# Performance work log

Measured on AMD Instinct MI355X. Metric: run time of the kernel, lower is better.

The kernel has to match this reference:

```python
import jax, jax.numpy as jnp
import numpy as np

B, N, D, M, H = 8, 576, 512, 16, 8
DH = D // H
K = int(D * 0.1)  # sparsity_ratio=0.1 -> k=51
EPS = 1e-5


def setup_inputs() -> dict:
    key = jax.random.key(0)
    ks = jax.random.split(key, 12)
    s = 0.02
    return {
        "F_clean": jax.random.normal(ks[0], (B, N, D), jnp.float32),
        "in_proj_w": jax.random.normal(ks[1], (3 * D, D), jnp.float32) * s,
        "in_proj_b": jnp.zeros((3 * D,), jnp.float32),
        "out_proj_w": jax.random.normal(ks[2], (D, D), jnp.float32) * s,
        "out_proj_b": jnp.zeros((D,), jnp.float32),
        "w1": jax.random.normal(ks[3], (D, D), jnp.float32) * s,
        "b1": jnp.zeros((D,), jnp.float32),
        "ln_g": jnp.ones((D,), jnp.float32),
        "ln_b": jnp.zeros((D,), jnp.float32),
        "w2": jax.random.normal(ks[4], (M, D), jnp.float32) * s,
        "b2": jnp.zeros((M,), jnp.float32),
        "templates": jax.random.normal(ks[5], (M, D), jnp.float32),
    }


def reference(F_clean, in_proj_w, in_proj_b, out_proj_w, out_proj_b,
              w1, b1, ln_g, ln_b, w2, b2, templates):
    # --- self attention (torch MultiheadAttention, batch_first, eval mode) ---
    qkv = F_clean @ in_proj_w.T + in_proj_b              # [B,N,3D]
    q, k_, v = jnp.split(qkv, 3, axis=-1)
    def heads(t):
        return t.reshape(B, N, H, DH).transpose(0, 2, 1, 3)  # [B,H,N,dh]
    q, k_, v = heads(q), heads(k_), heads(v)
    scores = jnp.einsum('bhqd,bhkd->bhqk', q, k_) / jnp.sqrt(jnp.float32(DH))
    attn = jax.nn.softmax(scores, axis=-1)
    o = jnp.einsum('bhqk,bhkd->bhqd', attn, v).transpose(0, 2, 1, 3).reshape(B, N, D)
    attn_out = o @ out_proj_w.T + out_proj_b

    F_enh = F_clean + attn_out

    # --- decompose_mlp: Linear -> LayerNorm -> GELU(exact) -> Linear ---
    h = F_enh @ w1.T + b1
    mu = jnp.mean(h, axis=-1, keepdims=True)
    var = jnp.var(h, axis=-1, keepdims=True)
    h = (h - mu) / jnp.sqrt(var + EPS) * ln_g + ln_b
    h = jax.nn.gelu(h, approximate=False)
    components = h @ w2.T + b2                           # [B,N,M]

    # --- outer product: Q[b,n,d,m] = F[b,n,d] * templates[m,d] * comp[b,n,m] ---
    Q = F_clean[:, :, :, None] * templates.T[None, None, :, :] * components[:, :, None, :]

    # --- top-k sparsify along D for each (b,n,m) row ---
    Qr = Q.transpose(0, 1, 3, 2).reshape(B * N * M, D)
    _, topk_idx = jax.lax.top_k(jnp.abs(Qr), K)
    rows = jnp.arange(B * N * M)[:, None]
    mask = jnp.zeros_like(Qr).at[rows, topk_idx].set(1.0)
    Q_sparse = (Qr * mask).reshape(B, N, M, D).transpose(0, 1, 3, 2)
    return Q_sparse
```

## Files before the change

kernel.cpp:

```cpp
#include <hip/hip_runtime.h>
#include <math.h>

#define NNB   576
#define BNR   4608
#define KSEL  51

typedef unsigned short u16;
typedef __attribute__((ext_vector_type(8))) short bf16x8;
typedef __attribute__((ext_vector_type(4))) float f32x4;

__device__ __forceinline__ u16 f2bf(float f) {
    unsigned u = __float_as_uint(f);
    return (u16)((u + 0x8000u) >> 16);
}
__device__ __forceinline__ unsigned pack2(float a, float b) {
    unsigned ua = __float_as_uint(a), ub = __float_as_uint(b);
    return ((ua + 0x8000u) >> 16) | ((ub + 0x8000u) & 0xffff0000u);
}
__device__ __forceinline__ void load_lds16(const void* gp, void* lp) {
    __builtin_amdgcn_global_load_lds((const __attribute__((address_space(1))) void*)gp,
                                     (__attribute__((address_space(3))) void*)lp, 16, 0, 0);
}
__device__ __forceinline__ int dpp_red_add_i(int v) {
    v += __builtin_amdgcn_update_dpp(0, v, 0x111, 0xf, 0xf, true);
    v += __builtin_amdgcn_update_dpp(0, v, 0x112, 0xf, 0xf, true);
    v += __builtin_amdgcn_update_dpp(0, v, 0x114, 0xf, 0xf, true);
    v += __builtin_amdgcn_update_dpp(0, v, 0x118, 0xf, 0xf, true);
    v += __builtin_amdgcn_update_dpp(0, v, 0x142, 0xa, 0xf, true);
    v += __builtin_amdgcn_update_dpp(0, v, 0x143, 0xc, 0xf, true);
    return __builtin_amdgcn_readlane(v, 63);
}
__device__ __forceinline__ float dpp_red_add_f(float x) {
    x += __int_as_float(__builtin_amdgcn_update_dpp(0, __float_as_int(x), 0x111, 0xf, 0xf, true));
    x += __int_as_float(__builtin_amdgcn_update_dpp(0, __float_as_int(x), 0x112, 0xf, 0xf, true));
    x += __int_as_float(__builtin_amdgcn_update_dpp(0, __float_as_int(x), 0x114, 0xf, 0xf, true));
    x += __int_as_float(__builtin_amdgcn_update_dpp(0, __float_as_int(x), 0x118, 0xf, 0xf, true));
    x += __int_as_float(__builtin_amdgcn_update_dpp(0, __float_as_int(x), 0x142, 0xa, 0xf, true));
    x += __int_as_float(__builtin_amdgcn_update_dpp(0, __float_as_int(x), 0x143, 0xc, 0xf, true));
    return __int_as_float(__builtin_amdgcn_readlane(__float_as_int(x), 63));
}

__global__ __launch_bounds__(256)
void cast_bf16(const float* __restrict__ F, const float* __restrict__ ipw,
               const float* __restrict__ opw, const float* __restrict__ w1,
               u16* __restrict__ Fb, u16* __restrict__ ipwb,
               u16* __restrict__ opwb, u16* __restrict__ w1b)
{
    size_t i4 = ((size_t)blockIdx.x * 256 + threadIdx.x) * 4;
    const float* src; u16* dst; size_t off;
    if      (i4 < 2359296) { src = F;   dst = Fb;   off = i4; }
    else if (i4 < 3145728) { src = ipw; dst = ipwb; off = i4 - 2359296; }
    else if (i4 < 3407872) { src = opw; dst = opwb; off = i4 - 3145728; }
    else                   { src = w1;  dst = w1b;  off = i4 - 3407872; }
    float4 v = *(const float4*)(src + off);
    uint2 o; o.x = pack2(v.x, v.y); o.y = pack2(v.z, v.w);
    *(uint2*)(dst + off) = o;
}

template<bool RESID, bool OUT_BF16, bool QSCALE>
__global__ __launch_bounds__(256)
void gemm_mfma64(const u16* __restrict__ A, const u16* __restrict__ Bw,
                 const float* __restrict__ bias, const float* __restrict__ res,
                 void* __restrict__ Cv, int Mr, int Nc, int Kd)
{
    __shared__ uint4 As4[512];
    __shared__ uint4 Bs4[1024];
    const int tid = threadIdx.x;
    const int lane = tid & 63, w = tid >> 6;
    const int wu = __builtin_amdgcn_readfirstlane(w);
    const int r16 = lane & 15, quad = lane >> 4;
    const int r0 = blockIdx.y << 6, c0 = blockIdx.x << 7;

    const u16* pA[2]; const u16* pB[4];
    #pragma unroll
    for (int rd = 0; rd < 2; ++rd) {
        const int c = (rd << 8) + tid;
        const int kb = c >> 8, g = (c >> 6) & 3, rr = (c >> 2) & 15, q = c & 3;
        pA[rd] = A + (size_t)(r0 + (g << 4) + rr) * Kd + (kb << 5) + (q << 3);
    }
    #pragma unroll
    for (int rd = 0; rd < 4; ++rd) {
        const int c = (rd << 8) + tid;
        const int kb = c >> 9, g = (c >> 6) & 7, rr = (c >> 2) & 15, q = c & 3;
        pB[rd] = Bw + (size_t)(c0 + (g << 4) + rr) * Kd + (kb << 5) + (q << 3);
    }

    f32x4 acc[4][2];
    #pragma unroll
    for (int i = 0; i < 4; ++i)
        #pragma unroll
        for (int j = 0; j < 2; ++j) acc[i][j] = (f32x4){0.f, 0.f, 0.f, 0.f};

    for (int kk = 0; kk < Kd; kk += 64) {
        __syncthreads();
        #pragma unroll
        for (int rd = 0; rd < 2; ++rd)
            load_lds16(pA[rd] + kk, (void*)(As4 + (rd << 8) + (wu << 6)));
        #pragma unroll
        for (int rd = 0; rd < 4; ++rd)
            load_lds16(pB[rd] + kk, (void*)(Bs4 + (rd << 8) + (wu << 6)));
        __syncthreads();
        #pragma unroll
        for (int kb = 0; kb < 2; ++kb) {
            bf16x8 af[4], bfr[2];
            #pragma unroll
            for (int i = 0; i < 4; ++i)
                af[i] = *(const bf16x8*)&As4[((kb * 4 + i) << 6) + (r16 << 2) + quad];
            #pragma unroll
            for (int j = 0; j < 2; ++j)
                bfr[j] = *(const bf16x8*)&Bs4[((kb * 8 + (w << 1) + j) << 6) + (r16 << 2) + quad];
            #pragma unroll
            for (int i = 0; i < 4; ++i)
                #pragma unroll
                for (int j = 0; j < 2; ++j)
                    acc[i][j] = __builtin_amdgcn_mfma_f32_16x16x32_bf16(af[i], bfr[j], acc[i][j], 0, 0, 0);
        }
    }

    float bcol[2], scl[2];
    #pragma unroll
    for (int j = 0; j < 2; ++j) {
        const int col = c0 + (w << 5) + (j << 4) + r16;
        bcol[j] = bias[col];
        scl[j] = (QSCALE && col < 512) ? 0.180336880111120426f : 1.0f;
    }
    #pragma unroll
    for (int i = 0; i < 4; ++i) {
        #pragma unroll
        for (int reg = 0; reg < 4; ++reg) {
            const int row = r0 + (i << 4) + (quad << 2) + reg;
            const size_t base = (size_t)row * Nc;
            #pragma unroll
            for (int j = 0; j < 2; ++j) {
                const int col = c0 + (w << 5) + (j << 4) + r16;
                float v = acc[i][j][reg] + bcol[j];
                if (RESID) v += res[base + col];
                if (QSCALE) v *= scl[j];
                if (OUT_BF16) ((u16*)Cv)[base + col] = f2bf(v);
                else          ((float*)Cv)[base + col] = v;
            }
        }
    }
}

template<bool RESID, bool OUT_BF16>
__global__ __launch_bounds__(256)
void gemm_6464(const u16* __restrict__ A, const u16* __restrict__ Bw,
               const float* __restrict__ bias, const float* __restrict__ res,
               void* __restrict__ Cv, int Mr, int Nc, int Kd)
{
    __shared__ uint4 As4[512];
    __shared__ uint4 Bs4[512];
    const int tid = threadIdx.x;
    const int lane = tid & 63, w = tid >> 6;
    const int wu = __builtin_amdgcn_readfirstlane(w);
    const int r16 = lane & 15, quad = lane >> 4;
    const int wy = w >> 1, wx = w & 1;
    const int r0 = blockIdx.y << 6, c0 = blockIdx.x << 6;

    const u16* pA[2]; const u16* pB[2];
    #pragma unroll
    for (int rd = 0; rd < 2; ++rd) {
        const int c = (rd << 8) + tid;
        const int kb = c >> 8, g = (c >> 6) & 3, rr = (c >> 2) & 15, q = c & 3;
        const int row = (g << 4) + rr;
        const int koff = (kb << 5) + (q << 3);
        pA[rd] = A  + (size_t)(r0 + row) * Kd + koff;
        pB[rd] = Bw + (size_t)(c0 + row) * Kd + koff;
    }

    f32x4 acc[2][2];
    #pragma unroll
    for (int i = 0; i < 2; ++i)
        #pragma unroll
        for (int j = 0; j < 2; ++j) acc[i][j] = (f32x4){0.f, 0.f, 0.f, 0.f};

    for (int kk = 0; kk < Kd; kk += 64) {
        __syncthreads();
        #pragma unroll
        for (int rd = 0; rd < 2; ++rd) {
            load_lds16(pA[rd] + kk, (void*)(As4 + (rd << 8) + (wu << 6)));
            load_lds16(pB[rd] + kk, (void*)(Bs4 + (rd << 8) + (wu << 6)));
        }
        __syncthreads();
        #pragma unroll
        for (int kb = 0; kb < 2; ++kb) {
            bf16x8 af[2], bfr[2];
            #pragma unroll
            for (int i = 0; i < 2; ++i)
                af[i] = *(const bf16x8*)&As4[((kb * 4 + (wy << 1) + i) << 6) + (r16 << 2) + quad];
            #pragma unroll
            for (int j = 0; j < 2; ++j)
                bfr[j] = *(const bf16x8*)&Bs4[((kb * 4 + (wx << 1) + j) << 6) + (r16 << 2) + quad];
            #pragma unroll
            for (int i = 0; i < 2; ++i)
                #pragma unroll
                for (int j = 0; j < 2; ++j)
                    acc[i][j] = __builtin_amdgcn_mfma_f32_16x16x32_bf16(af[i], bfr[j], acc[i][j], 0, 0, 0);
        }
    }

    float bcol[2];
    #pragma unroll
    for (int j = 0; j < 2; ++j) bcol[j] = bias[c0 + (wx << 5) + (j << 4) + r16];
    #pragma unroll
    for (int i = 0; i < 2; ++i) {
        #pragma unroll
        for (int reg = 0; reg < 4; ++reg) {
            const int row = r0 + (wy << 5) + (i << 4) + (quad << 2) + reg;
            const size_t base = (size_t)row * Nc;
            #pragma unroll
            for (int j = 0; j < 2; ++j) {
                const int col = c0 + (wx << 5) + (j << 4) + r16;
                float v = acc[i][j][reg] + bcol[j];
                if (RESID) v += res[base + col];
                if (OUT_BF16) ((u16*)Cv)[base + col] = f2bf(v);
                else          ((float*)Cv)[base + col] = v;
            }
        }
    }
}

__global__ __launch_bounds__(256)
void attn_mfma(const u16* __restrict__ qkv, u16* __restrict__ obuf)
{
    __shared__ uint4 Qf[512];
    __shared__ uint4 Kf[512];
    __shared__ u16  Vfs[4096];
    __shared__ u16  Pfs[4096];
    const int tid = threadIdx.x;
    const int lane = tid & 63, w = tid >> 6;
    const int wu = __builtin_amdgcn_readfirstlane(w);
    const int r16 = lane & 15, quad = lane >> 4;
    const int b = blockIdx.y >> 3, h = blockIdx.y & 7;
    const int i0 = blockIdx.x << 6;
    const u16* qb = qkv + (size_t)b * NNB * 1536 + h * 64;

    #pragma unroll
    for (int s = 0; s < 2; ++s) {
        const int linear = (s << 8) + tid;
        const int r = linear >> 3, q7 = linear & 7;
        uint4 v = *(const uint4*)(qb + (size_t)(i0 + r) * 1536 + (q7 << 3));
        Qf[(((q7 >> 2) * 4 + (r >> 4)) << 6) + ((r & 15) << 2) + (q7 & 3)] = v;
    }
    const u16* pK[2];
    #pragma unroll
    for (int rd = 0; rd < 2; ++rd) {
        const int c = (rd << 8) + tid;
        const int kb = c >> 8, g = (c >> 6) & 3, rr = (c >> 2) & 15, q = c & 3;
        pK[rd] = qb + 512 + (size_t)((g << 4) + rr) * 1536 + (kb << 5) + (q << 3);
    }
    const int vp = tid >> 3, vq7 = tid & 7;
    const int vj = vp << 1;
    const int vjl2 = (vj & 7) >> 1, vjq = (vj >> 3) & 3, vjkb = vj >> 5;

    float l_i[4] = {0.f, 0.f, 0.f, 0.f};
    f32x4 accO[4];
    #pragma unroll
    for (int f = 0; f < 4; ++f) accO[f] = (f32x4){0.f, 0.f, 0.f, 0.f};

    for (int j0 = 0; j0 < NNB; j0 += 64) {
        const u16* vbase = qb + 1024 + (size_t)(j0 + vj) * 1536 + (vq7 << 3);
        uint4 vA = *(const uint4*)vbase;
        uint4 vB = *(const uint4*)(vbase + 1536);
        __syncthreads();
        load_lds16(pK[0] + (size_t)j0 * 1536, (void*)(Kf + (wu << 6)));
        load_lds16(pK[1] + (size_t)j0 * 1536, (void*)(Kf + 256 + (wu << 6)));
        {
            const u16* ea = (const u16*)&vA;
            const u16* eb = (const u16*)&vB;
            unsigned* V32 = (unsigned*)Vfs;
            #pragma unroll
            for (int e = 0; e < 8; ++e) {
                const int d = (vq7 << 3) + e;
                const int g = d >> 4;
                const int ch = ((vjkb * 4 + g) << 6) + ((((d & 15) << 2) + vjq) ^ g);
                V32[(ch << 2) + vjl2] = (unsigned)ea[e] | ((unsigned)eb[e] << 16);
            }
        }
        __syncthreads();

        f32x4 accS[4];
        #pragma unroll
        for (int f = 0; f < 4; ++f) accS[f] = (f32x4){0.f, 0.f, 0.f, 0.f};
        #pragma unroll
        for (int kb = 0; kb < 2; ++kb) {
            bf16x8 aq = *(const bf16x8*)&Qf[((kb * 4 + w) << 6) + (r16 << 2) + quad];
            #pragma unroll
            for (int f = 0; f < 4; ++f) {
                bf16x8 bk = *(const bf16x8*)&Kf[((kb * 4 + f) << 6) + (r16 << 2) + quad];
                accS[f] = __builtin_amdgcn_mfma_f32_16x16x32_bf16(aq, bk, accS[f], 0, 0, 0);
            }
        }
        #pragma unroll
        for (int reg = 0; reg < 4; ++reg) {
            const float s0 = exp2f(accS[0][reg]);
            const float s1 = exp2f(accS[1][reg]);
            const float s2 = exp2f(accS[2][reg]);
            const float s3 = exp2f(accS[3][reg]);
            l_i[reg] += (s0 + s1) + (s2 + s3);
            const int m = (quad << 2) + reg;
            const int sm = ((m & 3) << 2) + (m >> 2);
            const float pv[4] = {s0, s1, s2, s3};
            #pragma unroll
            for (int f = 0; f < 4; ++f) {
                const int k = (f << 4) + r16;
                const int ch = (((k >> 5) * 4 + w) << 6) + (((k >> 3) & 3) << 4) + sm;
                Pfs[(ch << 3) + (k & 7)] = f2bf(pv[f]);
            }
        }
        #pragma unroll
        for (int kb = 0; kb < 2; ++kb) {
            bf16x8 ap = *(const bf16x8*)&Pfs[((((kb * 4 + w) << 6) + (quad << 4) + ((r16 & 3) << 2) + (r16 >> 2)) << 3)];
            #pragma unroll
            for (int f = 0; f < 4; ++f) {
                bf16x8 bv = *(const bf16x8*)&Vfs[((((kb * 4 + f) << 6) + (((r16 << 2) + quad) ^ f)) << 3)];
                accO[f] = __builtin_amdgcn_mfma_f32_16x16x32_bf16(ap, bv, accO[f], 0, 0, 0);
            }
        }
    }
    #pragma unroll
    for (int reg = 0; reg < 4; ++reg) {
        float l = l_i[reg];
        l += __shfl_xor(l, 1); l += __shfl_xor(l, 2);
        l += __shfl_xor(l, 4); l += __shfl_xor(l, 8);
        const float inv = 1.0f / l;
        const size_t row = (size_t)(b * NNB + i0 + (w << 4) + (quad << 2) + reg);
        #pragma unroll
        for (int f = 0; f < 4; ++f)
            obuf[row * 512 + (h << 6) + (f << 4) + r16] = f2bf(accO[f][reg] * inv);
    }
}

__global__ __launch_bounds__(256)
void outer_topk(const float* __restrict__ F, const float* __restrict__ hraw,
                const float* __restrict__ lng, const float* __restrict__ lnb,
                const float* __restrict__ w2, const float* __restrict__ b2,
                const float* __restrict__ T, float* __restrict__ out)
{
    const int bn = blockIdx.x;
    const int tid = threadIdx.x;
    const int lane = tid & 63, w = tid >> 6;
    __shared__ float Fr[512];
    __shared__ float Hr[512];
    __shared__ unsigned keyslots[4][4][64];
    __shared__ float redsm[8];

    if (tid < 128)
        *(float4*)&Fr[tid << 2] = *(const float4*)(F + (size_t)bn * 512 + (tid << 2));
    const float* hp = hraw + (size_t)bn * 512;
    float x0 = hp[tid], x1 = hp[tid + 256];
    float sw = dpp_red_add_f(x0 + x1);
    float sqw = dpp_red_add_f(x0 * x0 + x1 * x1);
    if (lane == 0) { redsm[w] = sw; redsm[4 + w] = sqw; }
    __syncthreads();
    const float s  = redsm[0] + redsm[1] + redsm[2] + redsm[3];
    const float sq = redsm[4] + redsm[5] + redsm[6] + redsm[7];
    const float mean = s * (1.0f / 512.0f);
    const float var  = sq * (1.0f / 512.0f) - mean * mean;
    const float rstd = rsqrtf(var + 1e-5f);
    float y = (x0 - mean) * rstd * lng[tid] + lnb[tid];
    Hr[tid] = 0.5f * y * (1.0f + erff(y * 0.70710678118654752f));
    y = (x1 - mean) * rstd * lng[tid + 256] + lnb[tid + 256];
    Hr[tid + 256] = 0.5f * y * (1.0f + erff(y * 0.70710678118654752f));
    __syncthreads();

    const int m0 = w << 2;
    float cm[4];
    #pragma unroll
    for (int mi = 0; mi < 4; ++mi) {
        const float* w2p = w2 + (size_t)(m0 + mi) * 512;
        float p = 0.f;
        #pragma unroll
        for (int t = 0; t < 8; ++t) p += Hr[lane + (t << 6)] * w2p[lane + (t << 6)];
        cm[mi] = dpp_red_add_f(p) + b2[m0 + mi];
    }

    unsigned u[4][8]; unsigned smask[4];
    #pragma unroll
    for (int mi = 0; mi < 4; ++mi) {
        smask[mi] = 0u;
        const float* Tp = T + (size_t)(m0 + mi) * 512;
        #pragma unroll
        for (int t = 0; t < 8; ++t) {
            float pp = Fr[lane + (t << 6)] * Tp[lane + (t << 6)];
            float pc = pp * cm[mi];
            const unsigned bits = __float_as_uint(pc);
            u[mi][t] = bits & 0x7fffffffu;
            smask[mi] |= (bits >> 31) << t;
        }
    }

    unsigned pref[4] = {0u, 0u, 0u, 0u};
    int cntP[4] = {512, 512, 512, 512};
    int U[4] = {0, 0, 0, 0};
    for (int bit = 30; bit >= 23; --bit) {
        const unsigned msk = 1u << bit;
        unsigned cand[4]; int cl[4];
        #pragma unroll
        for (int mi = 0; mi < 4; ++mi) {
            cand[mi] = pref[mi] | msk;
            int cc = 0;
            #pragma unroll
            for (int t = 0; t < 8; ++t) cc += (u[mi][t] >= cand[mi]) ? 1 : 0;
            cl[mi] = cc;
        }
        int cnt[4];
        #pragma unroll
        for (int mi = 0; mi < 4; ++mi) cnt[mi] = dpp_red_add_i(cl[mi]);
        #pragma unroll
        for (int mi = 0; mi < 4; ++mi) {
            if (cnt[mi] >= KSEL) { pref[mi] = cand[mi]; cntP[mi] = cnt[mi]; }
            else U[mi] = cnt[mi];
        }
    }
    int blo[4];
    #pragma unroll
    for (int mi = 0; mi < 4; ++mi) {
        int b = 23;
        while ((cntP[mi] - U[mi]) > 64 && b > 0) {
            --b;
            const unsigned cand = pref[mi] | (1u << b);
            int cc = 0;
            #pragma unroll
            for (int t = 0; t < 8; ++t) cc += (u[mi][t] >= cand) ? 1 : 0;
            const int cnt = dpp_red_add_i(cc);
            if (cnt >= KSEL) { pref[mi] = cand; cntP[mi] = cnt; } else U[mi] = cnt;
        }
        blo[mi] = b;
    }
    int need[4]; bool done[4];
    #pragma unroll
    for (int mi = 0; mi < 4; ++mi) {
        need[mi] = KSEL - U[mi];
        done[mi] = (need[mi] == cntP[mi] - U[mi]);
    }

    const unsigned long long lmask = (1ull << lane) - 1ull;
    unsigned kv[4] = {0u, 0u, 0u, 0u};
    #pragma unroll
    for (int mi = 0; mi < 4; ++mi) {
        if (done[mi]) continue;
        keyslots[w][mi][lane] = 0u;
        const int bl = blo[mi];
        const unsigned lowmask = (1u << bl) - 1u;
        int running = 0;
        #pragma unroll
        for (int t = 0; t < 8; ++t) {
            const bool tie = ((u[mi][t] ^ pref[mi]) >> bl) == 0u;
            const unsigned long long M = __ballot(tie);
            const int slot = running + __popcll(M & lmask);
            if (tie && slot < 64) {
                const unsigned key = ((u[mi][t] & lowmask) << 9) | (unsigned)(511 - ((t << 6) + lane));
                keyslots[w][mi][slot] = key;
            }
            running += __popcll(M);
        }
        kv[mi] = keyslots[w][mi][lane];
    }

    unsigned prefk[4] = {0u, 0u, 0u, 0u};
    for (int bb = 31; bb >= 0; --bb) {
        if (done[0] & done[1] & done[2] & done[3]) break;
        #pragma unroll
        for (int mi = 0; mi < 4; ++mi) {
            if (done[mi]) continue;
            const unsigned candk = prefk[mi] | (1u << bb);
            const int c = __popcll(__ballot(kv[mi] >= candk));
            if (c >= need[mi]) {
                prefk[mi] = candk;
                if (c == need[mi]) done[mi] = true;
            }
        }
    }

    float* ob = out + (size_t)bn * 8192 + m0;
    #pragma unroll
    for (int t = 0; t < 8; ++t) {
        const int d = (t << 6) + lane;
        float4 v;
        float* vv = &v.x;
        #pragma unroll
        for (int mi = 0; mi < 4; ++mi) {
            const unsigned uu = u[mi][t];
            const int bl = blo[mi];
            const bool tie = ((uu ^ pref[mi]) >> bl) == 0u;
            const unsigned key = ((uu & ((1u << bl) - 1u)) << 9) | (unsigned)(511 - d);
            const bool sel = (uu >= pref[mi] + (1u << bl)) || (tie && key >= prefk[mi]);
            const unsigned bits = uu | (((smask[mi] >> t) & 1u) << 31);
            vv[mi] = sel ? __uint_as_float(bits) : 0.0f;
        }
        *(float4*)(ob + (size_t)d * 16) = v;
    }
}

extern "C" void kernel_launch(void* const* d_in, const int* in_sizes, int n_in,
                              void* d_out, int out_size, void* d_ws, size_t ws_size,
                              hipStream_t stream)
{
    const float* F    = (const float*)d_in[0];
    const float* ipw  = (const float*)d_in[1];
    const float* ipb  = (const float*)d_in[2];
    const float* opw  = (const float*)d_in[3];
    const float* opb  = (const float*)d_in[4];
    const float* w1   = (const float*)d_in[5];
    const float* b1   = (const float*)d_in[6];
    const float* lng  = (const float*)d_in[7];
    const float* lnb  = (const float*)d_in[8];
    const float* w2   = (const float*)d_in[9];
    const float* b2   = (const float*)d_in[10];
    const float* tmpl = (const float*)d_in[11];

    char* wsb = (char*)d_ws;
    u16*   qkvb  = (u16*)wsb;
    u16*   obufb = (u16*)(wsb + 14155776);
    u16*   fenhb = (u16*)(wsb + 18874368);
    float* hbuf  = (float*)(wsb + 23592960);
    u16*   Fbf   = (u16*)(wsb + 33030144);
    u16*   ipwbf = (u16*)(wsb + 37748736);
    u16*   opwbf = (u16*)(wsb + 39321600);
    u16*   w1bf  = (u16*)(wsb + 39845888);

    cast_bf16<<<3584, 256, 0, stream>>>(F, ipw, opw, w1, Fbf, ipwbf, opwbf, w1bf);
    gemm_mfma64<false, true, true><<<dim3(12, 72), 256, 0, stream>>>(Fbf, ipwbf, ipb, nullptr, qkvb, BNR, 1536, 512);
    attn_mfma<<<dim3(9, 64), 256, 0, stream>>>(qkvb, obufb);
    gemm_6464<true, true><<<dim3(8, 72), 256, 0, stream>>>(obufb, opwbf, opb, F, fenhb, BNR, 512, 512);
    gemm_6464<false, false><<<dim3(8, 72), 256, 0, stream>>>(fenhb, w1bf, b1, nullptr, hbuf, BNR, 512, 512);
    outer_topk<<<4608, 256, 0, stream>>>(F, hbuf, lng, lnb, w2, b2, tmpl, (float*)d_out);
}
```

Measured before the change: 290.2 us.

## Fuse fp32-to-bf16 casts into GEMM loads and speed up top-k radix search

Removes the separate cast_bf16 kernel. The QKV and projection GEMMs now load fp32 operands directly, pack them to bf16 in registers and store them to LDS, which saves one launch plus a write and read of the bf16 copies. The top-k threshold search now starts at the row maximum's exponent and steps down one exponent at a time using ballot and popcount instead of DPP add reductions. The attention grid axes are also swapped. In exchange, the GEMM loads go through registers instead of direct-to-LDS loads and read twice the bytes, and the exponent-stepping loop varies in length from row to row.

```diff
diff --git a/kernel.cpp b/kernel.cpp
--- a/kernel.cpp
+++ b/kernel.cpp
@@ -20,15 +20,6 @@
 __device__ __forceinline__ void load_lds16(const void* gp, void* lp) {
     __builtin_amdgcn_global_load_lds((const __attribute__((address_space(1))) void*)gp,
                                      (__attribute__((address_space(3))) void*)lp, 16, 0, 0);
-}
-__device__ __forceinline__ int dpp_red_add_i(int v) {
-    v += __builtin_amdgcn_update_dpp(0, v, 0x111, 0xf, 0xf, true);
-    v += __builtin_amdgcn_update_dpp(0, v, 0x112, 0xf, 0xf, true);
-    v += __builtin_amdgcn_update_dpp(0, v, 0x114, 0xf, 0xf, true);
-    v += __builtin_amdgcn_update_dpp(0, v, 0x118, 0xf, 0xf, true);
-    v += __builtin_amdgcn_update_dpp(0, v, 0x142, 0xa, 0xf, true);
-    v += __builtin_amdgcn_update_dpp(0, v, 0x143, 0xc, 0xf, true);
-    return __builtin_amdgcn_readlane(v, 63);
 }
 __device__ __forceinline__ float dpp_red_add_f(float x) {
     x += __int_as_float(__builtin_amdgcn_update_dpp(0, __float_as_int(x), 0x111, 0xf, 0xf, true));
@@ -39,39 +30,30 @@
     x += __int_as_float(__builtin_amdgcn_update_dpp(0, __float_as_int(x), 0x143, 0xc, 0xf, true));
     return __int_as_float(__builtin_amdgcn_readlane(__float_as_int(x), 63));
 }
+__device__ __forceinline__ unsigned dpp_red_max_u(unsigned x) {
+    unsigned o;
+    o = (unsigned)__builtin_amdgcn_update_dpp(0, (int)x, 0x111, 0xf, 0xf, true); x = x > o ? x : o;
+    o = (unsigned)__builtin_amdgcn_update_dpp(0, (int)x, 0x112, 0xf, 0xf, true); x = x > o ? x : o;
+    o = (unsigned)__builtin_amdgcn_update_dpp(0, (int)x, 0x114, 0xf, 0xf, true); x = x > o ? x : o;
+    o = (unsigned)__builtin_amdgcn_update_dpp(0, (int)x, 0x118, 0xf, 0xf, true); x = x > o ? x : o;
+    o = (unsigned)__builtin_amdgcn_update_dpp(0, (int)x, 0x142, 0xa, 0xf, true); x = x > o ? x : o;
+    o = (unsigned)__builtin_amdgcn_update_dpp(0, (int)x, 0x143, 0xc, 0xf, true); x = x > o ? x : o;
+    return (unsigned)__builtin_amdgcn_readlane((int)x, 63);
+}
 
 __global__ __launch_bounds__(256)
-void cast_bf16(const float* __restrict__ F, const float* __restrict__ ipw,
-               const float* __restrict__ opw, const float* __restrict__ w1,
-               u16* __restrict__ Fb, u16* __restrict__ ipwb,
-               u16* __restrict__ opwb, u16* __restrict__ w1b)
-{
-    size_t i4 = ((size_t)blockIdx.x * 256 + threadIdx.x) * 4;
-    const float* src; u16* dst; size_t off;
-    if      (i4 < 2359296) { src = F;   dst = Fb;   off = i4; }
-    else if (i4 < 3145728) { src = ipw; dst = ipwb; off = i4 - 2359296; }
-    else if (i4 < 3407872) { src = opw; dst = opwb; off = i4 - 3145728; }
-    else                   { src = w1;  dst = w1b;  off = i4 - 3407872; }
-    float4 v = *(const float4*)(src + off);
-    uint2 o; o.x = pack2(v.x, v.y); o.y = pack2(v.z, v.w);
-    *(uint2*)(dst + off) = o;
-}
-
-template<bool RESID, bool OUT_BF16, bool QSCALE>
-__global__ __launch_bounds__(256)
-void gemm_mfma64(const u16* __restrict__ A, const u16* __restrict__ Bw,
-                 const float* __restrict__ bias, const float* __restrict__ res,
-                 void* __restrict__ Cv, int Mr, int Nc, int Kd)
+void gemm_qkv(const float* __restrict__ A, const float* __restrict__ Bw,
+              const float* __restrict__ bias, u16* __restrict__ Cv,
+              int Nc, int Kd)
 {
     __shared__ uint4 As4[512];
     __shared__ uint4 Bs4[1024];
     const int tid = threadIdx.x;
     const int lane = tid & 63, w = tid >> 6;
-    const int wu = __builtin_amdgcn_readfirstlane(w);
     const int r16 = lane & 15, quad = lane >> 4;
     const int r0 = blockIdx.y << 6, c0 = blockIdx.x << 7;
 
-    const u16* pA[2]; const u16* pB[4];
+    const float* pA[2]; const float* pB[4];
     #pragma unroll
     for (int rd = 0; rd < 2; ++rd) {
         const int c = (rd << 8) + tid;
@@ -92,13 +74,32 @@
         for (int j = 0; j < 2; ++j) acc[i][j] = (f32x4){0.f, 0.f, 0.f, 0.f};
 
     for (int kk = 0; kk < Kd; kk += 64) {
+        float4 a0[2], a1[2], b0[4], b1[4];
+        #pragma unroll
+        for (int rd = 0; rd < 2; ++rd) {
+            a0[rd] = *(const float4*)(pA[rd] + kk);
+            a1[rd] = *(const float4*)(pA[rd] + kk + 4);
+        }
+        #pragma unroll
+        for (int rd = 0; rd < 4; ++rd) {
+            b0[rd] = *(const float4*)(pB[rd] + kk);
+            b1[rd] = *(const float4*)(pB[rd] + kk + 4);
+        }
         __syncthreads();
         #pragma unroll
-        for (int rd = 0; rd < 2; ++rd)
-            load_lds16(pA[rd] + kk, (void*)(As4 + (rd << 8) + (wu << 6)));
-        #pragma unroll
-        for (int rd = 0; rd < 4; ++rd)
-            load_lds16(pB[rd] + kk, (void*)(Bs4 + (rd << 8) + (wu << 6)));
+        for (int rd = 0; rd < 2; ++rd) {
+            uint4 pk;
+            pk.x = pack2(a0[rd].x, a0[rd].y); pk.y = pack2(a0[rd].z, a0[rd].w);
+            pk.z = pack2(a1[rd].x, a1[rd].y); pk.w = pack2(a1[rd].z, a1[rd].w);
+            As4[(rd << 8) + tid] = pk;
+        }
+        #pragma unroll
+        for (int rd = 0; rd < 4; ++rd) {
+            uint4 pk;
+            pk.x = pack2(b0[rd].x, b0[rd].y); pk.y = pack2(b0[rd].z, b0[rd].w);
+            pk.z = pack2(b1[rd].x, b1[rd].y); pk.w = pack2(b1[rd].z, b1[rd].w);
+            Bs4[(rd << 8) + tid] = pk;
+        }
         __syncthreads();
         #pragma unroll
         for (int kb = 0; kb < 2; ++kb) {
@@ -122,7 +123,7 @@
     for (int j = 0; j < 2; ++j) {
         const int col = c0 + (w << 5) + (j << 4) + r16;
         bcol[j] = bias[col];
-        scl[j] = (QSCALE && col < 512) ? 0.180336880111120426f : 1.0f;
+        scl[j] = (col < 512) ? 0.180336880111120426f : 1.0f;
     }
     #pragma unroll
     for (int i = 0; i < 4; ++i) {
@@ -133,11 +134,7 @@
             #pragma unroll
             for (int j = 0; j < 2; ++j) {
                 const int col = c0 + (w << 5) + (j << 4) + r16;
-                float v = acc[i][j][reg] + bcol[j];
-                if (RESID) v += res[base + col];
-                if (QSCALE) v *= scl[j];
-                if (OUT_BF16) ((u16*)Cv)[base + col] = f2bf(v);
-                else          ((float*)Cv)[base + col] = v;
+                Cv[base + col] = f2bf((acc[i][j][reg] + bcol[j]) * scl[j]);
             }
         }
     }
@@ -145,9 +142,9 @@
 
 template<bool RESID, bool OUT_BF16>
 __global__ __launch_bounds__(256)
-void gemm_6464(const u16* __restrict__ A, const u16* __restrict__ Bw,
+void gemm_6464(const u16* __restrict__ A, const float* __restrict__ Bw,
                const float* __restrict__ bias, const float* __restrict__ res,
-               void* __restrict__ Cv, int Mr, int Nc, int Kd)
+               void* __restrict__ Cv, int Nc, int Kd)
 {
     __shared__ uint4 As4[512];
     __shared__ uint4 Bs4[512];
@@ -158,7 +155,7 @@
     const int wy = w >> 1, wx = w & 1;
     const int r0 = blockIdx.y << 6, c0 = blockIdx.x << 6;
 
-    const u16* pA[2]; const u16* pB[2];
+    const u16* pA[2]; const float* pB[2];
     #pragma unroll
     for (int rd = 0; rd < 2; ++rd) {
         const int c = (rd << 8) + tid;
@@ -176,11 +173,22 @@
         for (int j = 0; j < 2; ++j) acc[i][j] = (f32x4){0.f, 0.f, 0.f, 0.f};
 
     for (int kk = 0; kk < Kd; kk += 64) {
+        float4 b0[2], b1[2];
+        #pragma unroll
+        for (int rd = 0; rd < 2; ++rd) {
+            b0[rd] = *(const float4*)(pB[rd] + kk);
+            b1[rd] = *(const float4*)(pB[rd] + kk + 4);
+        }
         __syncthreads();
         #pragma unroll
+        for (int rd = 0; rd < 2; ++rd)
+            load_lds16(pA[rd] + kk, (void*)(As4 + (rd << 8) + (wu << 6)));
+        #pragma unroll
         for (int rd = 0; rd < 2; ++rd) {
-            load_lds16(pA[rd] + kk, (void*)(As4 + (rd << 8) + (wu << 6)));
-            load_lds16(pB[rd] + kk, (void*)(Bs4 + (rd << 8) + (wu << 6)));
+            uint4 pk;
+            pk.x = pack2(b0[rd].x, b0[rd].y); pk.y = pack2(b0[rd].z, b0[rd].w);
+            pk.z = pack2(b1[rd].x, b1[rd].y); pk.w = pack2(b1[rd].z, b1[rd].w);
+            Bs4[(rd << 8) + tid] = pk;
         }
         __syncthreads();
         #pragma unroll
@@ -232,8 +240,8 @@
     const int lane = tid & 63, w = tid >> 6;
     const int wu = __builtin_amdgcn_readfirstlane(w);
     const int r16 = lane & 15, quad = lane >> 4;
-    const int b = blockIdx.y >> 3, h = blockIdx.y & 7;
-    const int i0 = blockIdx.x << 6;
+    const int b = blockIdx.x >> 3, h = blockIdx.x & 7;
+    const int i0 = blockIdx.y << 6;
     const u16* qb = qkv + (size_t)b * NNB * 1536 + h * 64;
 
     #pragma unroll
@@ -391,27 +399,26 @@
         }
     }
 
-    unsigned pref[4] = {0u, 0u, 0u, 0u};
-    int cntP[4] = {512, 512, 512, 512};
-    int U[4] = {0, 0, 0, 0};
-    for (int bit = 30; bit >= 23; --bit) {
-        const unsigned msk = 1u << bit;
-        unsigned cand[4]; int cl[4];
+    unsigned pref[4], cand[4];
+    int cntP[4], U[4];
+    bool ad[4];
+    #pragma unroll
+    for (int mi = 0; mi < 4; ++mi) {
+        unsigned mx = u[mi][0];
+        #pragma unroll
+        for (int t = 1; t < 8; ++t) mx = mx > u[mi][t] ? mx : u[mi][t];
+        cand[mi] = dpp_red_max_u(mx) & 0xff800000u;
+        pref[mi] = 0u; cntP[mi] = 512; U[mi] = 0; ad[mi] = false;
+    }
+    while (!(ad[0] & ad[1] & ad[2] & ad[3])) {
         #pragma unroll
         for (int mi = 0; mi < 4; ++mi) {
-            cand[mi] = pref[mi] | msk;
-            int cc = 0;
-            #pragma unroll
-            for (int t = 0; t < 8; ++t) cc += (u[mi][t] >= cand[mi]) ? 1 : 0;
-            cl[mi] = cc;
-        }
-        int cnt[4];
-        #pragma unroll
-        for (int mi = 0; mi < 4; ++mi) cnt[mi] = dpp_red_add_i(cl[mi]);
-        #pragma unroll
-        for (int mi = 0; mi < 4; ++mi) {
-            if (cnt[mi] >= KSEL) { pref[mi] = cand[mi]; cntP[mi] = cnt[mi]; }
-            else U[mi] = cnt[mi];
+            if (ad[mi]) continue;
+            int cnt = 0;
+            #pragma unroll
+            for (int t = 0; t < 8; ++t) cnt += __popcll(__ballot(u[mi][t] >= cand[mi]));
+            if (cnt >= KSEL) { pref[mi] = cand[mi]; cntP[mi] = cnt; ad[mi] = true; }
+            else             { U[mi] = cnt; cand[mi] -= (1u << 23); }
         }
     }
     int blo[4];
@@ -420,12 +427,11 @@
         int b = 23;
         while ((cntP[mi] - U[mi]) > 64 && b > 0) {
             --b;
-            const unsigned cand = pref[mi] | (1u << b);
-            int cc = 0;
-            #pragma unroll
-            for (int t = 0; t < 8; ++t) cc += (u[mi][t] >= cand) ? 1 : 0;
-            const int cnt = dpp_red_add_i(cc);
-            if (cnt >= KSEL) { pref[mi] = cand; cntP[mi] = cnt; } else U[mi] = cnt;
+            const unsigned cc2 = pref[mi] | (1u << b);
+            int cnt = 0;
+            #pragma unroll
+            for (int t = 0; t < 8; ++t) cnt += __popcll(__ballot(u[mi][t] >= cc2));
+            if (cnt >= KSEL) { pref[mi] = cc2; cntP[mi] = cnt; } else U[mi] = cnt;
         }
         blo[mi] = b;
     }
@@ -516,15 +522,10 @@
     u16*   obufb = (u16*)(wsb + 14155776);
     u16*   fenhb = (u16*)(wsb + 18874368);
     float* hbuf  = (float*)(wsb + 23592960);
-    u16*   Fbf   = (u16*)(wsb + 33030144);
-    u16*   ipwbf = (u16*)(wsb + 37748736);
-    u16*   opwbf = (u16*)(wsb + 39321600);
-    u16*   w1bf  = (u16*)(wsb + 39845888);
-
-    cast_bf16<<<3584, 256, 0, stream>>>(F, ipw, opw, w1, Fbf, ipwbf, opwbf, w1bf);
-    gemm_mfma64<false, true, true><<<dim3(12, 72), 256, 0, stream>>>(Fbf, ipwbf, ipb, nullptr, qkvb, BNR, 1536, 512);
-    attn_mfma<<<dim3(9, 64), 256, 0, stream>>>(qkvb, obufb);
-    gemm_6464<true, true><<<dim3(8, 72), 256, 0, stream>>>(obufb, opwbf, opb, F, fenhb, BNR, 512, 512);
-    gemm_6464<false, false><<<dim3(8, 72), 256, 0, stream>>>(fenhb, w1bf, b1, nullptr, hbuf, BNR, 512, 512);
+
+    gemm_qkv<<<dim3(12, 72), 256, 0, stream>>>(F, ipw, ipb, qkvb, 1536, 512);
+    attn_mfma<<<dim3(64, 9), 256, 0, stream>>>(qkvb, obufb);
+    gemm_6464<true, true><<<dim3(8, 72), 256, 0, stream>>>(obufb, opw, opb, F, fenhb, 512, 512);
+    gemm_6464<false, false><<<dim3(8, 72), 256, 0, stream>>>(fenhb, w1, b1, nullptr, hbuf, 512, 512);
     outer_topk<<<4608, 256, 0, stream>>>(F, hbuf, lng, lnb, w2, b2, tmpl, (float*)d_out);
 }
```

New measurement: 292.0 us. Within noise of the previous version (+0.6%).
